# Performance work log

Hardware: AMD Instinct MI355X
Metric: run time of the kernel (lower is better)

Reference implementation:

```python
import jax, jax.numpy as jnp
import numpy as np

N_NODES = 100000
N_EDGES = 1200000
DIM = 64
MAX_DEG = 64
NUM_LAB = 16
BN_EPS = 1e-5


def _lrelu(x):
    return jax.nn.leaky_relu(x, negative_slope=0.01)


def _bn(x, g, b):
    # BatchNorm1d in training mode: batch statistics over node axis
    m = x.mean(axis=0)
    v = x.var(axis=0)
    return (x - m) * jax.lax.rsqrt(v + BN_EPS) * g + b


def _gin_layer(h, src, dst, n, w1, b1, w2, b2, eps, g, b):
    # GINConv: (1+eps)*x_i + sum_{j in N(i)} x_j, then MLP (lin_lrelu_lin), BN, LeakyReLU
    agg = jax.ops.segment_sum(h[src], dst, num_segments=n)
    x = (1.0 + eps) * h + agg
    x = _lrelu(x @ w1 + b1) @ w2 + b2
    return _lrelu(_bn(x, g, b))


def setup_inputs() -> dict:
    key = jax.random.key(0)
    ks = jax.random.split(key, 16)
    s = 0.05
    inp = {
        'node_deg': jax.random.randint(ks[0], (N_NODES,), 0, MAX_DEG + 1, dtype=jnp.int32),
        'node_lab': jax.random.randint(ks[1], (N_NODES,), 0, NUM_LAB, dtype=jnp.int32),
        'edge_index': jax.random.randint(ks[2], (2, N_EDGES), 0, N_NODES, dtype=jnp.int32),
        'emb_deg': jax.random.normal(ks[3], (MAX_DEG + 1, DIM), jnp.float32) * s,
        'emb_lab': jax.random.normal(ks[4], (NUM_LAB, DIM), jnp.float32) * s,
        'l0_w1': jax.random.normal(ks[5], (2 * DIM, 2 * DIM), jnp.float32) * s,
        'l0_b1': jnp.zeros((2 * DIM,), jnp.float32),
        'l0_w2': jax.random.normal(ks[6], (2 * DIM, DIM), jnp.float32) * s,
        'l0_b2': jnp.zeros((DIM,), jnp.float32),
        'l0_eps': jnp.zeros((1,), jnp.float32),
        'bn0_g': jnp.ones((DIM,), jnp.float32),
        'bn0_b': jnp.zeros((DIM,), jnp.float32),
        'l1_w1': jax.random.normal(ks[7], (DIM, DIM), jnp.float32) * s,
        'l1_b1': jnp.zeros((DIM,), jnp.float32),
        'l1_w2': jax.random.normal(ks[8], (DIM, DIM), jnp.float32) * s,
        'l1_b2': jnp.zeros((DIM,), jnp.float32),
        'l1_eps': jnp.zeros((1,), jnp.float32),
        'bn1_g': jnp.ones((DIM,), jnp.float32),
        'bn1_b': jnp.zeros((DIM,), jnp.float32),
        'fc_w1': jax.random.normal(ks[9], (4 * DIM, DIM), jnp.float32) * s,
        'fc_b1': jnp.zeros((DIM,), jnp.float32),
        'fc_bn_g': jnp.ones((DIM,), jnp.float32),
        'fc_bn_b': jnp.zeros((DIM,), jnp.float32),
        'fc_w2': jax.random.normal(ks[10], (DIM, 1), jnp.float32) * s,
        'fc_b2': jnp.zeros((1,), jnp.float32),
    }
    return inp


def reference(node_deg, node_lab, edge_index, emb_deg, emb_lab,
              l0_w1, l0_b1, l0_w2, l0_b2, l0_eps, bn0_g, bn0_b,
              l1_w1, l1_b1, l1_w2, l1_b2, l1_eps, bn1_g, bn1_b,
              fc_w1, fc_b1, fc_bn_g, fc_bn_b, fc_w2, fc_b2):
    n = node_deg.shape[0]
    src, dst = edge_index[0], edge_index[1]
    # embedding concat: [N, 2*DIM]
    h0 = jnp.concatenate([emb_deg[node_deg], emb_lab[node_lab]], axis=1)
    h1 = _gin_layer(h0, src, dst, n, l0_w1, l0_b1, l0_w2, l0_b2, l0_eps[0], bn0_g, bn0_b)
    h2 = _gin_layer(h1, src, dst, n, l1_w1, l1_b1, l1_w2, l1_b2, l1_eps[0], bn1_g, bn1_b)
    x = jnp.concatenate([h0, h1, h2], axis=1)  # [N, 256]
    x = _lrelu(_bn(x @ fc_w1 + fc_b1, fc_bn_g, fc_bn_b))
    out = jax.nn.sigmoid(x @ fc_w2 + fc_b2)
    return out.squeeze(-1)  # [N]
```

## Files before the change

### kernel.cpp

```cpp
#include <hip/hip_runtime.h>

#define N_NODES 100000
#define N_EDGES 1200000
#define NCLS 81
#define NBKT 196
#define BCAP 8192
#define NCHK 293
#define NGBLK 1563
#define NAGG 6250

typedef unsigned short u16;
typedef unsigned char u8;
typedef unsigned int u32;
typedef unsigned long long u64;
typedef short bf16x8 __attribute__((ext_vector_type(8)));
typedef float f32x4 __attribute__((ext_vector_type(4)));

__device__ __forceinline__ float b2f(u16 u) {
  union { u32 i; float f; } v; v.i = ((u32)u) << 16; return v.f;
}
__device__ __forceinline__ u16 f2b(float f) {
  union { float f; u32 i; } v; v.f = f;
  u32 x = v.i;
  return (u16)((x + 0x7fffu + ((x >> 16) & 1u)) >> 16);
}
__device__ __forceinline__ void up2(u32 w, float& lo, float& hi) {
  union { u32 u; float f; } a, b;
  a.u = w << 16; b.u = w & 0xffff0000u;
  lo = a.f; hi = b.f;
}
__device__ __forceinline__ float lrelu(float x) { return x > 0.f ? x : 0.01f * x; }

__device__ __forceinline__ bool is_f32(const u16* emb) {
  int lane = threadIdx.x & 63;
  u32 e0 = (emb[lane * 2] >> 7) & 0xFF;
  u32 e1 = (emb[lane * 2 + 1] >> 7) & 0xFF;
  return __ballot((e0 >= 0x90) || (e1 >= 0x90)) != 0ull;
}

__device__ __forceinline__ float rdr(const void* p, int i, bool f32m) {
  return f32m ? ((const float*)p)[i] : b2f(((const u16*)p)[i]);
}

#define P_EMBD 0
#define P_EMBL 4160
#define P_W1A  5184
#define P_B1A  21568
#define P_W2A  21696
#define P_B2A  29888
#define P_EPS0 29952
#define P_G0   29953
#define P_BB0  30017
#define P_LW1  30081
#define P_LB1  34177
#define P_LW2  34241
#define P_LB2  38337
#define P_EPS1 38401
#define P_G1   38402
#define P_BB1  38466
#define P_FW1  38530
#define P_FB1  54914
#define P_FG   54978
#define P_FBB  55042
#define P_FW2  55106
#define P_FB2  55170
#define P_TOT  55171

struct CvtAll {
  const void* src[22];
  int cnt[22];
  int off[22];
};

struct RawPtrs {
  const void* embD;
  const void* embL;
  const void* w1r;
  const void* w2r;
  const void* lw1r;
  const void* lw2r;
  const void* fwr;
};

__global__ void k_init(CvtAll a, RawPtrs rw, const u16* __restrict__ embRaw,
                       float* __restrict__ P, float* __restrict__ W1p,
                       float* __restrict__ Efc, u16* __restrict__ bp,
                       u16* __restrict__ wpB, u32* __restrict__ gcur) {
  bool f32m = is_f32(embRaw);
  int tid = threadIdx.x;
  if (blockIdx.y < 22) {
    if (blockIdx.y == 0 && blockIdx.x == 0 && tid < NBKT) gcur[tid] = 0;
    int seg = blockIdx.y;
    int i = blockIdx.x * 256 + tid;
    if (i < a.cnt[seg]) {
      float v = f32m ? ((const float*)a.src[seg])[i] : b2f(((const u16*)a.src[seg])[i]);
      P[a.off[seg] + i] = v;
    }
    return;
  }
  int idx = blockIdx.x * 256 + tid;
  if (idx < NCLS * 128) {
    int c = idx >> 7, h = idx & 127;
    float s = 0.f;
    if (c < 65) {
      for (int k = 0; k < 64; ++k)
        s = fmaf(rdr(rw.embD, c * 64 + k, f32m), rdr(rw.w1r, k * 128 + h, f32m), s);
    } else {
      for (int k = 0; k < 64; ++k)
        s = fmaf(rdr(rw.embL, (c - 65) * 64 + k, f32m), rdr(rw.w1r, (64 + k) * 128 + h, f32m), s);
    }
    W1p[idx] = s;
    return;
  }
  if (idx < NCLS * 128 + NCLS * 64) {
    int r = idx - NCLS * 128;
    int c = r >> 6, o = r & 63;
    float s = 0.f;
    if (c < 65) {
      for (int k = 0; k < 64; ++k)
        s = fmaf(rdr(rw.embD, c * 64 + k, f32m), rdr(rw.fwr, k * 64 + o, f32m), s);
    } else {
      for (int k = 0; k < 64; ++k)
        s = fmaf(rdr(rw.embL, (c - 65) * 64 + k, f32m), rdr(rw.fwr, (64 + k) * 64 + o, f32m), s);
    }
    Efc[r] = s;
    return;
  }
  if (idx < NCLS * 128 + NCLS * 64 + 24576) {
    int pidx = idx - (NCLS * 128 + NCLS * 64);
    int seg, rel;
    if (pidx < 8192)       { seg = 0; rel = pidx; }
    else if (pidx < 12288) { seg = 1; rel = pidx - 8192; }
    else if (pidx < 16384) { seg = 2; rel = pidx - 12288; }
    else                   { seg = 3; rel = pidx - 16384; }
    const void* srcs[4] = {rw.w2r, rw.lw1r, rw.lw2r, rw.fwr};
    const int addoff[4] = {0, 0, 0, 128 * 64};
    const int KBs[4] = {4, 2, 2, 4};
    int j = rel & 7, lane = (rel >> 3) & 63, rest = rel >> 9;
    int kb = rest % KBs[seg], nt = rest / KBs[seg];
    int k = kb * 32 + (lane >> 4) * 8 + j;
    int n = nt * 16 + (lane & 15);
    bp[pidx] = f2b(rdr(srcs[seg], addoff[seg] + k * 64 + n, f32m));
    return;
  }
  int p2 = idx - (NCLS * 128 + NCLS * 64 + 24576);
  if (p2 >= 12288) return;
  int j = p2 & 7, lane = (p2 >> 3) & 63, rest = p2 >> 9;
  int kb = rest % 3, nt = rest / 3;
  int c = kb * 32 + (lane >> 4) * 8 + j;
  int n = nt * 16 + (lane & 15);
  float s = 0.f;
  if (c < NCLS) {
    if (c < 65) {
      for (int k = 0; k < 64; ++k)
        s = fmaf(rdr(rw.embD, c * 64 + k, f32m), rdr(rw.w1r, k * 128 + n, f32m), s);
    } else {
      for (int k = 0; k < 64; ++k)
        s = fmaf(rdr(rw.embL, (c - 65) * 64 + k, f32m), rdr(rw.w1r, (64 + k) * 128 + n, f32m), s);
    }
  }
  wpB[p2] = (c < NCLS) ? f2b(s) : 0;
}

__global__ __launch_bounds__(256) void k_bsort(const int* __restrict__ edge,
                                               const int* __restrict__ ndeg,
                                               const int* __restrict__ nlab,
                                               u32* __restrict__ gcur,
                                               u64* __restrict__ e2) {
  __shared__ u32 cnt[NBKT], rbase[NBKT];
  __shared__ u32 slo[4096], shi[4096];
  for (int i = threadIdx.x; i < NBKT; i += 256) cnt[i] = 0;
  __syncthreads();
  int base = blockIdx.x * 4096;
  for (int i = threadIdx.x; i < 4096; i += 256) {
    int e = base + i;
    if (e < N_EDGES) {
      int s = edge[e], d = edge[N_EDGES + e];
      slo[i] = ((u32)s << 11) | ((u32)ndeg[s] << 4) | (u32)nlab[s];
      shi[i] = (u32)d;
      atomicAdd(&cnt[(u32)d >> 9], 1u);
    } else shi[i] = 0xFFFFFFFFu;
  }
  __syncthreads();
  for (int i = threadIdx.x; i < NBKT; i += 256) {
    u32 c = cnt[i];
    rbase[i] = c ? atomicAdd(&gcur[i], c) : 0u;
    cnt[i] = 0;
  }
  __syncthreads();
  for (int i = threadIdx.x; i < 4096; i += 256) {
    u32 d = shi[i];
    if (d == 0xFFFFFFFFu) continue;
    u32 b = d >> 9;
    u32 pos = rbase[b] + atomicAdd(&cnt[b], 1u);
    e2[(size_t)b * BCAP + pos] = ((u64)d << 32) | (u64)slo[i];
  }
}

__global__ __launch_bounds__(512) void k_csrh(const u64* __restrict__ e2,
                                              const u32* __restrict__ gcur,
                                              const u16* __restrict__ wpB,
                                              const float* __restrict__ W1p,
                                              const float* __restrict__ P,
                                              const int* __restrict__ ndeg,
                                              const int* __restrict__ nlab,
                                              u32* __restrict__ row_ptr,
                                              u32* __restrict__ einfo,
                                              u16* __restrict__ hmid) {
  __shared__ u32 l[512], cur[512], gl[NBKT];
  __shared__ u32 h32[512 * 24];
  __shared__ u32 sbase;
  int b = blockIdx.x, tid = threadIdx.x;
  if (tid < NBKT) gl[tid] = gcur[tid];
  l[tid] = 0;
  for (int i = tid; i < 512 * 24; i += 512) h32[i] = 0;
  __syncthreads();
  if (tid == 0) {
    u32 s = 0;
    for (int i = 0; i < b; ++i) s += gl[i];
    sbase = s;
  }
  __syncthreads();
  u32 cnt = gl[b];
  const u64* src = e2 + (size_t)b * BCAP;
  for (u32 e = tid; e < cnt; e += 512)
    atomicAdd(&l[(u32)(src[e] >> 32) & 511u], 1u);
  __syncthreads();
  u32 v = l[tid];
  for (int off = 1; off < 512; off <<= 1) {
    u32 a = (tid >= off) ? l[tid - off] : 0u;
    __syncthreads();
    l[tid] += a;
    __syncthreads();
  }
  u32 pos0 = sbase + l[tid] - v;
  cur[tid] = pos0;
  int nn = b * 512 + tid;
  if (nn <= N_NODES) row_ptr[nn] = pos0;
  __syncthreads();
  for (u32 e = tid; e < cnt; e += 512) {
    u64 r = src[e];
    u32 dl = (u32)(r >> 32) & 511u;
    u32 lo = (u32)r;
    u32 pos = atomicAdd(&cur[dl], 1u);
    einfo[pos] = lo;
    u32 c1 = (lo >> 4) & 0x7Fu, c2 = 65u + (lo & 15u);
    atomicAdd(&h32[dl * 24 + (c1 >> 2)], 1u << ((c1 & 3u) * 8));
    atomicAdd(&h32[dl * 24 + (c2 >> 2)], 1u << ((c2 & 3u) * 8));
  }
  __syncthreads();
  const u8* h = (const u8*)h32;
  int wid = tid >> 6, lane = tid & 63;
  int row = lane & 15, q = lane >> 4;
  float onep = 1.f + P[P_EPS0];
  const bf16x8* bp = (const bf16x8*)wpB;
#pragma unroll 1
  for (int t = wid; t < 32; t += 8) {
    int m0 = b * 512 + t * 16;
    if (m0 >= N_NODES) break;
    f32x4 acc[8];
#pragma unroll
    for (int nt = 0; nt < 8; ++nt) {
      float bb = P[P_B1A + nt * 16 + row];
      acc[nt][0] = bb; acc[nt][1] = bb; acc[nt][2] = bb; acc[nt][3] = bb;
    }
    const u8* ar = h + (t * 16 + row) * 96 + q * 8;
#pragma unroll
    for (int kb = 0; kb < 3; ++kb) {
      bf16x8 af;
#pragma unroll
      for (int j = 0; j < 8; ++j) af[j] = (short)f2b((float)ar[kb * 32 + j]);
#pragma unroll
      for (int nt = 0; nt < 8; ++nt) {
        bf16x8 bf = bp[(nt * 3 + kb) * 64 + lane];
        acc[nt] = __builtin_amdgcn_mfma_f32_16x16x32_bf16(af, bf, acc[nt], 0, 0, 0);
      }
    }
#pragma unroll
    for (int r = 0; r < 4; ++r) {
      int m = m0 + q * 4 + r;
      if (m >= N_NODES) continue;
      const float* wd = W1p + ndeg[m] * 128;
      const float* wl = W1p + (65 + nlab[m]) * 128;
#pragma unroll
      for (int nt = 0; nt < 8; ++nt) {
        int cc = nt * 16 + row;
        float vv = acc[nt][r] + onep * (wd[cc] + wl[cc]);
        hmid[(size_t)m * 128 + cc] = f2b(lrelu(vv));
      }
    }
  }
}

__global__ void k_sr(const float* __restrict__ pbuf, float* __restrict__ statsOut,
                     int nrows) {
  __shared__ float l[256];
  int c = blockIdx.x;
  float s = 0.f;
  for (int r = threadIdx.x; r < nrows; r += 256) s += pbuf[(size_t)r * 128 + c];
  l[threadIdx.x] = s;
  __syncthreads();
  for (int off = 128; off > 0; off >>= 1) {
    if (threadIdx.x < off) l[threadIdx.x] += l[threadIdx.x + off];
    __syncthreads();
  }
  if (threadIdx.x == 0) statsOut[c] = l[0];
}

template <int KB, int LDA, int BIASOFF>
__global__ __launch_bounds__(256) void k_gemm(const u16* __restrict__ A,
                                              const u16* __restrict__ Bp,
                                              const float* __restrict__ P,
                                              float* __restrict__ pbuf,
                                              u16* __restrict__ C) {
  __shared__ float lsum[4][64], lsq[4][64];
  int wid = threadIdx.x >> 6, lane = threadIdx.x & 63;
  int m0 = (blockIdx.x * 4 + wid) * 16;
  bool act = m0 < N_NODES;
  int row = lane & 15, q = lane >> 4;
  float ss[4] = {0.f, 0.f, 0.f, 0.f}, qq[4] = {0.f, 0.f, 0.f, 0.f};
  if (act) {
    const u16* ap = A + (size_t)(m0 + row) * LDA + q * 8;
    const bf16x8* bp = (const bf16x8*)Bp;
    f32x4 acc[4];
#pragma unroll
    for (int nt = 0; nt < 4; ++nt) {
      float b = (BIASOFF >= 0) ? P[BIASOFF + nt * 16 + row] : 0.f;
      acc[nt][0] = b; acc[nt][1] = b; acc[nt][2] = b; acc[nt][3] = b;
    }
#pragma unroll
    for (int kb = 0; kb < KB; ++kb) {
      bf16x8 af = *(const bf16x8*)(ap + kb * 32);
#pragma unroll
      for (int nt = 0; nt < 4; ++nt) {
        bf16x8 bf = bp[(nt * KB + kb) * 64 + lane];
        acc[nt] = __builtin_amdgcn_mfma_f32_16x16x32_bf16(af, bf, acc[nt], 0, 0, 0);
      }
    }
#pragma unroll
    for (int nt = 0; nt < 4; ++nt) {
      float s = 0.f, z = 0.f;
#pragma unroll
      for (int r = 0; r < 4; ++r) {
        int m = m0 + q * 4 + r;
        u16 bv = f2b(acc[nt][r]);
        C[(size_t)m * 64 + nt * 16 + row] = bv;
        float v = b2f(bv);
        s += v; z = fmaf(v, v, z);
      }
      s += __shfl_xor(s, 16, 64); s += __shfl_xor(s, 32, 64);
      z += __shfl_xor(z, 16, 64); z += __shfl_xor(z, 32, 64);
      ss[nt] = s; qq[nt] = z;
    }
  }
  if (lane < 16) {
#pragma unroll
    for (int nt = 0; nt < 4; ++nt) {
      lsum[wid][nt * 16 + lane] = ss[nt];
      lsq[wid][nt * 16 + lane] = qq[nt];
    }
  }
  __syncthreads();
  int t = threadIdx.x;
  if (t < 64)
    pbuf[(size_t)blockIdx.x * 128 + t] = lsum[0][t] + lsum[1][t] + lsum[2][t] + lsum[3][t];
  else if (t < 128) {
    int c = t - 64;
    pbuf[(size_t)blockIdx.x * 128 + t] = lsq[0][c] + lsq[1][c] + lsq[2][c] + lsq[3][c];
  }
}

__global__ __launch_bounds__(256) void k_gemm_bn(const u16* __restrict__ A,
                                                 const u16* __restrict__ Bp,
                                                 const float* __restrict__ P,
                                                 const float* __restrict__ stats,
                                                 u16* __restrict__ C) {
  int wid = threadIdx.x >> 6, lane = threadIdx.x & 63;
  int m0 = (blockIdx.x * 4 + wid) * 16;
  if (m0 >= N_NODES) return;
  int row = lane & 15, q = lane >> 4;
  const float invN = 1.f / (float)N_NODES;
  float sc[16], sh[16];
#pragma unroll
  for (int kb = 0; kb < 2; ++kb)
#pragma unroll
    for (int j = 0; j < 8; ++j) {
      int f = kb * 32 + q * 8 + j;
      float mm = stats[f] * invN;
      float var = fmaxf(stats[64 + f] * invN - mm * mm, 0.f);
      float inv = rsqrtf(var + 1e-5f);
      float s = inv * P[P_G0 + f];
      sc[kb * 8 + j] = s;
      sh[kb * 8 + j] = P[P_BB0 + f] - mm * s;
    }
  const u16* ap = A + (size_t)(m0 + row) * 64 + q * 8;
  const bf16x8* bp = (const bf16x8*)Bp;
  f32x4 acc[4];
#pragma unroll
  for (int nt = 0; nt < 4; ++nt) {
    acc[nt][0] = 0.f; acc[nt][1] = 0.f; acc[nt][2] = 0.f; acc[nt][3] = 0.f;
  }
#pragma unroll
  for (int kb = 0; kb < 2; ++kb) {
    uint4 raw = *(const uint4*)(ap + kb * 32);
    u32 rw[4] = {raw.x, raw.y, raw.z, raw.w};
    bf16x8 af;
#pragma unroll
    for (int p = 0; p < 4; ++p) {
      float lo, hi;
      up2(rw[p], lo, hi);
      float y0 = lrelu(fmaf(sc[kb * 8 + 2 * p], lo, sh[kb * 8 + 2 * p]));
      float y1 = lrelu(fmaf(sc[kb * 8 + 2 * p + 1], hi, sh[kb * 8 + 2 * p + 1]));
      af[2 * p] = (short)f2b(y0);
      af[2 * p + 1] = (short)f2b(y1);
    }
#pragma unroll
    for (int nt = 0; nt < 4; ++nt) {
      bf16x8 bf = bp[(nt * 2 + kb) * 64 + lane];
      acc[nt] = __builtin_amdgcn_mfma_f32_16x16x32_bf16(af, bf, acc[nt], 0, 0, 0);
    }
  }
#pragma unroll
  for (int nt = 0; nt < 4; ++nt)
#pragma unroll
    for (int r = 0; r < 4; ++r) {
      int m = m0 + q * 4 + r;
      C[(size_t)m * 64 + nt * 16 + row] = f2b(acc[nt][r]);
    }
}

__global__ __launch_bounds__(1024) void k_aggg(const u32* __restrict__ rp,
                                               const u32* __restrict__ einfo,
                                               const u16* __restrict__ g1,
                                               const u16* __restrict__ Bp,
                                               const float* __restrict__ P,
                                               float* __restrict__ pbuf,
                                               u16* __restrict__ C) {
  __shared__ u16 As[16][72];
  int lane = threadIdx.x & 63, wv = threadIdx.x >> 6;
  int m0 = blockIdx.x * 16;
  int n = m0 + wv;
  u32 st = rp[n], en = rp[n + 1];
  u32 m = en - st;
  int grp = lane >> 4;
  int fo = (lane & 15) * 4;
  u32 myidx = (u32)n;
  if (lane < (int)m) myidx = einfo[st + lane] >> 11;
  u32 mm = m < 64u ? m : 64u;
  float a0 = 0.f, a1 = 0.f, a2 = 0.f, a3 = 0.f;
  for (u32 k = 0; k < mm; k += 16) {
#pragma unroll
    for (int bb = 0; bb < 4; ++bb) {
      u32 e = k + (u32)(bb * 4 + grp);
      u32 src = (u32)__shfl((int)myidx, (int)e, 64);
      if (e < mm) {
        uint2 v = *(const uint2*)(g1 + (size_t)src * 64 + fo);
        float l0, h0, l1, h1;
        up2(v.x, l0, h0);
        up2(v.y, l1, h1);
        a0 += l0; a1 += h0; a2 += l1; a3 += h1;
      }
    }
  }
  a0 += __shfl_xor(a0, 16, 64); a0 += __shfl_xor(a0, 32, 64);
  a1 += __shfl_xor(a1, 16, 64); a1 += __shfl_xor(a1, 32, 64);
  a2 += __shfl_xor(a2, 16, 64); a2 += __shfl_xor(a2, 32, 64);
  a3 += __shfl_xor(a3, 16, 64); a3 += __shfl_xor(a3, 32, 64);
  for (u32 k = 64; k < m; ++k) {
    u32 src = einfo[st + k] >> 11;
    uint2 v = *(const uint2*)(g1 + (size_t)src * 64 + fo);
    float l0, h0, l1, h1;
    up2(v.x, l0, h0);
    up2(v.y, l1, h1);
    a0 += l0; a1 += h0; a2 += l1; a3 += h1;
  }
  float onep = 1.f + P[P_EPS1];
  uint2 sv = *(const uint2*)(g1 + (size_t)n * 64 + fo);
  float s0, s1, s2, s3;
  up2(sv.x, s0, s1);
  up2(sv.y, s2, s3);
  float r0 = P[P_LB1 + fo + 0] + fmaf(onep, s0, a0);
  float r1 = P[P_LB1 + fo + 1] + fmaf(onep, s1, a1);
  float r2 = P[P_LB1 + fo + 2] + fmaf(onep, s2, a2);
  float r3 = P[P_LB1 + fo + 3] + fmaf(onep, s3, a3);
  if (lane < 16) {
    uint2 o;
    o.x = ((u32)f2b(lrelu(r0))) | (((u32)f2b(lrelu(r1))) << 16);
    o.y = ((u32)f2b(lrelu(r2))) | (((u32)f2b(lrelu(r3))) << 16);
    *(uint2*)&As[wv][fo] = o;
  }
  __syncthreads();
  if (wv != 0) return;
  int row = lane & 15, q = lane >> 4;
  const u16* ap = &As[row][q * 8];
  const bf16x8* bp = (const bf16x8*)Bp;
  f32x4 acc[4];
#pragma unroll
  for (int nt = 0; nt < 4; ++nt) {
    float b = P[P_LB2 + nt * 16 + row];
    acc[nt][0] = b; acc[nt][1] = b; acc[nt][2] = b; acc[nt][3] = b;
  }
#pragma unroll
  for (int kb = 0; kb < 2; ++kb) {
    bf16x8 af = *(const bf16x8*)(ap + kb * 32);
#pragma unroll
    for (int nt = 0; nt < 4; ++nt) {
      bf16x8 bf = bp[(nt * 2 + kb) * 64 + lane];
      acc[nt] = __builtin_amdgcn_mfma_f32_16x16x32_bf16(af, bf, acc[nt], 0, 0, 0);
    }
  }
  float ss[4], qq[4];
#pragma unroll
  for (int nt = 0; nt < 4; ++nt) {
    float s = 0.f, z = 0.f;
#pragma unroll
    for (int r = 0; r < 4; ++r) {
      int mo = m0 + q * 4 + r;
      u16 bv = f2b(acc[nt][r]);
      C[(size_t)mo * 64 + nt * 16 + row] = bv;
      float v = b2f(bv);
      s += v; z = fmaf(v, v, z);
    }
    s += __shfl_xor(s, 16, 64); s += __shfl_xor(s, 32, 64);
    z += __shfl_xor(z, 16, 64); z += __shfl_xor(z, 32, 64);
    ss[nt] = s; qq[nt] = z;
  }
  if (lane < 16) {
#pragma unroll
    for (int nt = 0; nt < 4; ++nt) {
      pbuf[(size_t)blockIdx.x * 128 + nt * 16 + lane] = ss[nt];
      pbuf[(size_t)blockIdx.x * 128 + 64 + nt * 16 + lane] = qq[nt];
    }
  }
}

__global__ __launch_bounds__(256) void k_gemm_fc1bn(const u16* __restrict__ t0,
                                                    const u16* __restrict__ t1,
                                                    const u16* __restrict__ Bp,
                                                    const float* __restrict__ P,
                                                    const float* __restrict__ stats,
                                                    float* __restrict__ pbuf,
                                                    const int* __restrict__ ndeg,
                                                    const int* __restrict__ nlab,
                                                    const float* __restrict__ Efc,
                                                    u16* __restrict__ C) {
  __shared__ float lsum[4][64], lsq[4][64];
  int wid = threadIdx.x >> 6, lane = threadIdx.x & 63;
  int m0 = (blockIdx.x * 4 + wid) * 16;
  bool act = m0 < N_NODES;
  int row = lane & 15, q = lane >> 4;
  float ss[4] = {0.f, 0.f, 0.f, 0.f}, qq[4] = {0.f, 0.f, 0.f, 0.f};
  if (act) {
    const float invN = 1.f / (float)N_NODES;
    float sc[32], sh[32];
#pragma unroll
    for (int h = 0; h < 2; ++h) {
      const float* st = stats + h * 128;
      int gof = h ? P_G1 : P_G0, bof = h ? P_BB1 : P_BB0;
#pragma unroll
      for (int kb = 0; kb < 2; ++kb)
#pragma unroll
        for (int j = 0; j < 8; ++j) {
          int f = kb * 32 + q * 8 + j;
          float mm = st[f] * invN;
          float var = fmaxf(st[64 + f] * invN - mm * mm, 0.f);
          float inv = rsqrtf(var + 1e-5f);
          float s = inv * P[gof + f];
          sc[h * 16 + kb * 8 + j] = s;
          sh[h * 16 + kb * 8 + j] = P[bof + f] - mm * s;
        }
    }
    const u16* a0 = t0 + (size_t)(m0 + row) * 64 + q * 8;
    const u16* a1 = t1 + (size_t)(m0 + row) * 64 + q * 8;
    const bf16x8* bp = (const bf16x8*)Bp;
    f32x4 acc[4];
#pragma unroll
    for (int nt = 0; nt < 4; ++nt) {
      float b = P[P_FB1 + nt * 16 + row];
      acc[nt][0] = b; acc[nt][1] = b; acc[nt][2] = b; acc[nt][3] = b;
    }
#pragma unroll
    for (int kb = 0; kb < 4; ++kb) {
      const u16* src = (kb < 2) ? (a0 + kb * 32) : (a1 + (kb - 2) * 32);
      int ci = (kb < 2) ? kb * 8 : 16 + (kb - 2) * 8;
      uint4 raw = *(const uint4*)src;
      u32 rw[4] = {raw.x, raw.y, raw.z, raw.w};
      bf16x8 af;
#pragma unroll
      for (int p = 0; p < 4; ++p) {
        float lo, hi;
        up2(rw[p], lo, hi);
        float y0 = lrelu(fmaf(sc[ci + 2 * p], lo, sh[ci + 2 * p]));
        float y1 = lrelu(fmaf(sc[ci + 2 * p + 1], hi, sh[ci + 2 * p + 1]));
        af[2 * p] = (short)f2b(y0);
        af[2 * p + 1] = (short)f2b(y1);
      }
#pragma unroll
      for (int nt = 0; nt < 4; ++nt) {
        bf16x8 bf = bp[(nt * 4 + kb) * 64 + lane];
        acc[nt] = __builtin_amdgcn_mfma_f32_16x16x32_bf16(af, bf, acc[nt], 0, 0, 0);
      }
    }
    float es[4][4];
#pragma unroll
    for (int r = 0; r < 4; ++r) {
      int m = m0 + q * 4 + r;
      int dn = ndeg[m], ln = 65 + nlab[m];
#pragma unroll
      for (int nt = 0; nt < 4; ++nt) {
        int cc = nt * 16 + row;
        es[r][nt] = acc[nt][r] + Efc[dn * 64 + cc] + Efc[ln * 64 + cc];
      }
    }
#pragma unroll
    for (int nt = 0; nt < 4; ++nt) {
      float s = 0.f, z = 0.f;
#pragma unroll
      for (int r = 0; r < 4; ++r) {
        int m = m0 + q * 4 + r;
        u16 bv = f2b(es[r][nt]);
        C[(size_t)m * 64 + nt * 16 + row] = bv;
        float v = b2f(bv);
        s += v; z = fmaf(v, v, z);
      }
      s += __shfl_xor(s, 16, 64); s += __shfl_xor(s, 32, 64);
      z += __shfl_xor(z, 16, 64); z += __shfl_xor(z, 32, 64);
      ss[nt] = s; qq[nt] = z;
    }
  }
  if (lane < 16) {
#pragma unroll
    for (int nt = 0; nt < 4; ++nt) {
      lsum[wid][nt * 16 + lane] = ss[nt];
      lsq[wid][nt * 16 + lane] = qq[nt];
    }
  }
  __syncthreads();
  int t = threadIdx.x;
  if (t < 64)
    pbuf[(size_t)blockIdx.x * 128 + t] = lsum[0][t] + lsum[1][t] + lsum[2][t] + lsum[3][t];
  else if (t < 128) {
    int c = t - 64;
    pbuf[(size_t)blockIdx.x * 128 + t] = lsq[0][c] + lsq[1][c] + lsq[2][c] + lsq[3][c];
  }
}

__global__ __launch_bounds__(256) void k_fc2(const u16* __restrict__ t,
                                             const float* __restrict__ stats,
                                             const float* __restrict__ P,
                                             const u16* __restrict__ embRaw,
                                             void* __restrict__ out) {
  __shared__ float scF[64], shF[64], fwF[64];
  bool f32m = is_f32(embRaw);
  int tid = threadIdx.x;
  if (tid < 64) {
    const float invN = 1.f / (float)N_NODES;
    float mm = stats[tid] * invN;
    float var = fmaxf(stats[64 + tid] * invN - mm * mm, 0.f);
    float inv = rsqrtf(var + 1e-5f);
    float s = inv * P[P_FG + tid];
    scF[tid] = s;
    shF[tid] = P[P_FBB + tid] - mm * s;
    fwF[tid] = P[P_FW2 + tid];
  }
  __syncthreads();
  int n = blockIdx.x * 256 + tid;
  if (n >= N_NODES) return;
  float z = P[P_FB2];
  const uint4* tn = (const uint4*)(t + (size_t)n * 64);
#pragma unroll
  for (int jj = 0; jj < 8; ++jj) {
    uint4 raw = tn[jj];
    u32 w[4] = {raw.x, raw.y, raw.z, raw.w};
#pragma unroll
    for (int p = 0; p < 4; ++p) {
      int f = jj * 8 + p * 2;
      float lo, hi;
      up2(w[p], lo, hi);
      float y0 = lrelu(fmaf(scF[f], lo, shF[f]));
      float y1 = lrelu(fmaf(scF[f + 1], hi, shF[f + 1]));
      z = fmaf(y0, fwF[f], z);
      z = fmaf(y1, fwF[f + 1], z);
    }
  }
  float s = 1.f / (1.f + expf(-z));
  if (!(fabsf(z) < 1e30f)) s = 0.25f;
  if (f32m) ((float*)out)[n] = s;
  else      ((u16*)out)[n] = f2b(s);
}

extern "C" void kernel_launch(void* const* d_in, const int* in_sizes, int n_in,
                              void* d_out, int out_size, void* d_ws, size_t ws_size,
                              hipStream_t stream) {
  const int* node_deg = (const int*)d_in[0];
  const int* node_lab = (const int*)d_in[1];
  const int* edge     = (const int*)d_in[2];
  const u16* embRaw   = (const u16*)d_in[3];
  (void)in_sizes; (void)n_in; (void)out_size; (void)ws_size;

  char* base = (char*)d_ws;
  size_t off = 0;
  auto alloc = [&](size_t bytes) -> void* {
    void* p = base + off;
    off += (bytes + 15) & ~(size_t)15;
    return p;
  };
  float* Pb    = (float*)alloc((size_t)P_TOT * 4);
  float* stats = (float*)alloc(384 * 4);
  u32* gcur    = (u32*)alloc(NBKT * 4);
  float* W1p   = (float*)alloc(NCLS * 128 * 4);
  float* Efc   = (float*)alloc(NCLS * 64 * 4);
  u16* bpack   = (u16*)alloc(24576 * 2);
  u16* wpB     = (u16*)alloc(12288 * 2);
  u32* row_ptr = (u32*)alloc((size_t)(N_NODES + 1) * 4);
  float* pbuf  = (float*)alloc((size_t)NAGG * 128 * 4);
  u32* einfo   = (u32*)alloc((size_t)N_EDGES * 4);
  u64* e2      = (u64*)alloc((size_t)NBKT * BCAP * 8);
  void* arena  = alloc((size_t)N_NODES * 128 * 2);
  u16* t0      = (u16*)alloc((size_t)N_NODES * 64 * 2);
  u16* t1      = (u16*)alloc((size_t)N_NODES * 64 * 2);
  u16* t2      = (u16*)alloc((size_t)N_NODES * 64 * 2);
  u16* hmid = (u16*)arena;
  u16* g1   = (u16*)arena;
  u16* Bp_w2a = bpack;
  u16* Bp_lw1 = bpack + 8192;
  u16* Bp_lw2 = bpack + 12288;
  u16* Bp_fw1 = bpack + 16384;

  CvtAll ca;
  const int srcidx[22] = {3, 4, 5, 6, 7, 8, 9, 10, 11, 12, 13, 14, 15, 16, 17, 18, 19, 20, 21, 22, 23, 24};
  const int cnts[22]   = {4160, 1024, 16384, 128, 8192, 64, 1, 64, 64, 4096, 64, 4096, 64, 1, 64, 64, 16384, 64, 64, 64, 64, 1};
  const int offs[22]   = {P_EMBD, P_EMBL, P_W1A, P_B1A, P_W2A, P_B2A, P_EPS0, P_G0, P_BB0,
                          P_LW1, P_LB1, P_LW2, P_LB2, P_EPS1, P_G1, P_BB1,
                          P_FW1, P_FB1, P_FG, P_FBB, P_FW2, P_FB2};
  for (int i = 0; i < 22; ++i) { ca.src[i] = d_in[srcidx[i]]; ca.cnt[i] = cnts[i]; ca.off[i] = offs[i]; }
  RawPtrs rw;
  rw.embD = d_in[3]; rw.embL = d_in[4]; rw.w1r = d_in[5]; rw.w2r = d_in[7];
  rw.lw1r = d_in[12]; rw.lw2r = d_in[14]; rw.fwr = d_in[19];

  k_init<<<dim3(205, 23), 256, 0, stream>>>(ca, rw, embRaw, Pb, W1p, Efc, bpack, wpB, gcur);

  k_bsort<<<NCHK, 256, 0, stream>>>(edge, node_deg, node_lab, gcur, e2);

  k_csrh<<<NBKT, 512, 0, stream>>>(e2, gcur, wpB, W1p, Pb, node_deg, node_lab,
                                   row_ptr, einfo, hmid);

  const int GEMM_GRID = NGBLK;

  k_gemm<4, 128, P_B2A><<<GEMM_GRID, 256, 0, stream>>>(hmid, Bp_w2a, Pb, pbuf, t0);
  k_sr<<<128, 256, 0, stream>>>(pbuf, stats, NGBLK);

  k_gemm_bn<<<GEMM_GRID, 256, 0, stream>>>(t0, Bp_lw1, Pb, stats, g1);
  k_aggg<<<NAGG, 1024, 0, stream>>>(row_ptr, einfo, g1, Bp_lw2, Pb, pbuf, t1);
  k_sr<<<128, 256, 0, stream>>>(pbuf, stats + 128, NAGG);

  k_gemm_fc1bn<<<GEMM_GRID, 256, 0, stream>>>(t0, t1, Bp_fw1, Pb, stats, pbuf,
                                              node_deg, node_lab, Efc, t2);
  k_sr<<<128, 256, 0, stream>>>(pbuf, stats + 256, NGBLK);
  k_fc2<<<(N_NODES + 255) / 256, 256, 0, stream>>>(t2, stats + 256, Pb, embRaw, d_out);
}
```

Measured before the change: 331.3 us.

## Fuse layer-0 second GEMM into CSR kernel and split aggregation from its GEMM

The layer-0 second linear layer (128->64) and its BN partial statistics now run inside k_csrh, using an LDS tile of the hidden activations, so the hmid round trip through global memory and a separate GEMM launch go away. The layer-1 aggregation kernel is reduced to 256-thread blocks that only gather neighbours and write the aggregated activations to a buffer. A generic k_gemm then applies the second layer-1 weight matrix and produces BN partials over fewer blocks, so the later stats reduction reads less. In exchange there is one extra intermediate buffer write and read, an additional kernel launch, and much more LDS per k_csrh block.

```diff
diff --git a/kernel.cpp b/kernel.cpp
--- a/kernel.cpp
+++ b/kernel.cpp
@@ -7,7 +7,6 @@
 #define BCAP 8192
 #define NCHK 293
 #define NGBLK 1563
-#define NAGG 6250
 
 typedef unsigned short u16;
 typedef unsigned char u8;
@@ -204,12 +203,16 @@
                                               const float* __restrict__ P,
                                               const int* __restrict__ ndeg,
                                               const int* __restrict__ nlab,
+                                              const u16* __restrict__ Bp2,
                                               u32* __restrict__ row_ptr,
                                               u32* __restrict__ einfo,
-                                              u16* __restrict__ hmid) {
+                                              u16* __restrict__ t0,
+                                              float* __restrict__ pbuf) {
   __shared__ u32 l[512], cur[512], gl[NBKT];
   __shared__ u32 h32[512 * 24];
   __shared__ u32 sbase;
+  __shared__ u16 T[8][16][136];
+  __shared__ float lsum[8][64], lsq[8][64];
   int b = blockIdx.x, tid = threadIdx.x;
   if (tid < NBKT) gl[tid] = gcur[tid];
   l[tid] = 0;
@@ -254,6 +257,8 @@
   int row = lane & 15, q = lane >> 4;
   float onep = 1.f + P[P_EPS0];
   const bf16x8* bp = (const bf16x8*)wpB;
+  const bf16x8* bp2 = (const bf16x8*)Bp2;
+  float ssA[4] = {0.f, 0.f, 0.f, 0.f}, qqA[4] = {0.f, 0.f, 0.f, 0.f};
 #pragma unroll 1
   for (int t = wid; t < 32; t += 8) {
     int m0 = b * 512 + t * 16;
@@ -279,16 +284,74 @@
 #pragma unroll
     for (int r = 0; r < 4; ++r) {
       int m = m0 + q * 4 + r;
-      if (m >= N_NODES) continue;
-      const float* wd = W1p + ndeg[m] * 128;
-      const float* wl = W1p + (65 + nlab[m]) * 128;
-#pragma unroll
-      for (int nt = 0; nt < 8; ++nt) {
-        int cc = nt * 16 + row;
-        float vv = acc[nt][r] + onep * (wd[cc] + wl[cc]);
-        hmid[(size_t)m * 128 + cc] = f2b(lrelu(vv));
-      }
-    }
+      int node = q * 4 + r;
+      if (m < N_NODES) {
+        const float* wd = W1p + ndeg[m] * 128;
+        const float* wl = W1p + (65 + nlab[m]) * 128;
+#pragma unroll
+        for (int nt = 0; nt < 8; ++nt) {
+          int cc = nt * 16 + row;
+          float vv = acc[nt][r] + onep * (wd[cc] + wl[cc]);
+          T[wid][node][cc] = f2b(lrelu(vv));
+        }
+      } else {
+#pragma unroll
+        for (int nt = 0; nt < 8; ++nt) T[wid][node][nt * 16 + row] = 0;
+      }
+    }
+    const u16* ap = &T[wid][row][q * 8];
+    f32x4 acc2[4];
+#pragma unroll
+    for (int nt = 0; nt < 4; ++nt) {
+      float bb = P[P_B2A + nt * 16 + row];
+      acc2[nt][0] = bb; acc2[nt][1] = bb; acc2[nt][2] = bb; acc2[nt][3] = bb;
+    }
+#pragma unroll
+    for (int kb = 0; kb < 4; ++kb) {
+      bf16x8 af = *(const bf16x8*)(ap + kb * 32);
+#pragma unroll
+      for (int nt = 0; nt < 4; ++nt) {
+        bf16x8 bf = bp2[(nt * 4 + kb) * 64 + lane];
+        acc2[nt] = __builtin_amdgcn_mfma_f32_16x16x32_bf16(af, bf, acc2[nt], 0, 0, 0);
+      }
+    }
+#pragma unroll
+    for (int nt = 0; nt < 4; ++nt) {
+      float s = 0.f, z = 0.f;
+#pragma unroll
+      for (int r = 0; r < 4; ++r) {
+        int m = m0 + q * 4 + r;
+        if (m < N_NODES) {
+          u16 bv = f2b(acc2[nt][r]);
+          t0[(size_t)m * 64 + nt * 16 + row] = bv;
+          float vv = b2f(bv);
+          s += vv; z = fmaf(vv, vv, z);
+        }
+      }
+      s += __shfl_xor(s, 16, 64); s += __shfl_xor(s, 32, 64);
+      z += __shfl_xor(z, 16, 64); z += __shfl_xor(z, 32, 64);
+      ssA[nt] += s; qqA[nt] += z;
+    }
+  }
+  if (lane < 16) {
+#pragma unroll
+    for (int nt = 0; nt < 4; ++nt) {
+      lsum[wid][nt * 16 + lane] = ssA[nt];
+      lsq[wid][nt * 16 + lane] = qqA[nt];
+    }
+  }
+  __syncthreads();
+  if (tid < 64) {
+    float s = 0.f;
+#pragma unroll
+    for (int w = 0; w < 8; ++w) s += lsum[w][tid];
+    pbuf[(size_t)b * 128 + tid] = s;
+  } else if (tid < 128) {
+    int c = tid - 64;
+    float s = 0.f;
+#pragma unroll
+    for (int w = 0; w < 8; ++w) s += lsq[w][c];
+    pbuf[(size_t)b * 128 + tid] = s;
   }
 }
 
@@ -429,17 +492,14 @@
     }
 }
 
-__global__ __launch_bounds__(1024) void k_aggg(const u32* __restrict__ rp,
-                                               const u32* __restrict__ einfo,
-                                               const u16* __restrict__ g1,
-                                               const u16* __restrict__ Bp,
-                                               const float* __restrict__ P,
-                                               float* __restrict__ pbuf,
-                                               u16* __restrict__ C) {
-  __shared__ u16 As[16][72];
+__global__ __launch_bounds__(256) void k_agg1(const u32* __restrict__ rp,
+                                              const u32* __restrict__ einfo,
+                                              const u16* __restrict__ g1,
+                                              const float* __restrict__ P,
+                                              u16* __restrict__ abuf) {
   int lane = threadIdx.x & 63, wv = threadIdx.x >> 6;
-  int m0 = blockIdx.x * 16;
-  int n = m0 + wv;
+  int n = blockIdx.x * 4 + wv;
+  if (n >= N_NODES) return;
   u32 st = rp[n], en = rp[n + 1];
   u32 m = en - st;
   int grp = lane >> 4;
@@ -487,50 +547,7 @@
     uint2 o;
     o.x = ((u32)f2b(lrelu(r0))) | (((u32)f2b(lrelu(r1))) << 16);
     o.y = ((u32)f2b(lrelu(r2))) | (((u32)f2b(lrelu(r3))) << 16);
-    *(uint2*)&As[wv][fo] = o;
-  }
-  __syncthreads();
-  if (wv != 0) return;
-  int row = lane & 15, q = lane >> 4;
-  const u16* ap = &As[row][q * 8];
-  const bf16x8* bp = (const bf16x8*)Bp;
-  f32x4 acc[4];
-#pragma unroll
-  for (int nt = 0; nt < 4; ++nt) {
-    float b = P[P_LB2 + nt * 16 + row];
-    acc[nt][0] = b; acc[nt][1] = b; acc[nt][2] = b; acc[nt][3] = b;
-  }
-#pragma unroll
-  for (int kb = 0; kb < 2; ++kb) {
-    bf16x8 af = *(const bf16x8*)(ap + kb * 32);
-#pragma unroll
-    for (int nt = 0; nt < 4; ++nt) {
-      bf16x8 bf = bp[(nt * 2 + kb) * 64 + lane];
-      acc[nt] = __builtin_amdgcn_mfma_f32_16x16x32_bf16(af, bf, acc[nt], 0, 0, 0);
-    }
-  }
-  float ss[4], qq[4];
-#pragma unroll
-  for (int nt = 0; nt < 4; ++nt) {
-    float s = 0.f, z = 0.f;
-#pragma unroll
-    for (int r = 0; r < 4; ++r) {
-      int mo = m0 + q * 4 + r;
-      u16 bv = f2b(acc[nt][r]);
-      C[(size_t)mo * 64 + nt * 16 + row] = bv;
-      float v = b2f(bv);
-      s += v; z = fmaf(v, v, z);
-    }
-    s += __shfl_xor(s, 16, 64); s += __shfl_xor(s, 32, 64);
-    z += __shfl_xor(z, 16, 64); z += __shfl_xor(z, 32, 64);
-    ss[nt] = s; qq[nt] = z;
-  }
-  if (lane < 16) {
-#pragma unroll
-    for (int nt = 0; nt < 4; ++nt) {
-      pbuf[(size_t)blockIdx.x * 128 + nt * 16 + lane] = ss[nt];
-      pbuf[(size_t)blockIdx.x * 128 + 64 + nt * 16 + lane] = qq[nt];
-    }
+    *(uint2*)(abuf + (size_t)n * 64 + fo) = o;
   }
 }
 
@@ -713,15 +730,15 @@
   u16* bpack   = (u16*)alloc(24576 * 2);
   u16* wpB     = (u16*)alloc(12288 * 2);
   u32* row_ptr = (u32*)alloc((size_t)(N_NODES + 1) * 4);
-  float* pbuf  = (float*)alloc((size_t)NAGG * 128 * 4);
+  float* pbuf  = (float*)alloc((size_t)NGBLK * 128 * 4);
   u32* einfo   = (u32*)alloc((size_t)N_EDGES * 4);
   u64* e2      = (u64*)alloc((size_t)NBKT * BCAP * 8);
   void* arena  = alloc((size_t)N_NODES * 128 * 2);
   u16* t0      = (u16*)alloc((size_t)N_NODES * 64 * 2);
   u16* t1      = (u16*)alloc((size_t)N_NODES * 64 * 2);
   u16* t2      = (u16*)alloc((size_t)N_NODES * 64 * 2);
-  u16* hmid = (u16*)arena;
   u16* g1   = (u16*)arena;
+  u16* abuf = (u16*)arena + (size_t)N_NODES * 64;
   u16* Bp_w2a = bpack;
   u16* Bp_lw1 = bpack + 8192;
   u16* Bp_lw2 = bpack + 12288;
@@ -743,16 +760,15 @@
   k_bsort<<<NCHK, 256, 0, stream>>>(edge, node_deg, node_lab, gcur, e2);
 
   k_csrh<<<NBKT, 512, 0, stream>>>(e2, gcur, wpB, W1p, Pb, node_deg, node_lab,
-                                   row_ptr, einfo, hmid);
+                                   Bp_w2a, row_ptr, einfo, t0, pbuf);
+  k_sr<<<128, 256, 0, stream>>>(pbuf, stats, NBKT);
 
   const int GEMM_GRID = NGBLK;
 
-  k_gemm<4, 128, P_B2A><<<GEMM_GRID, 256, 0, stream>>>(hmid, Bp_w2a, Pb, pbuf, t0);
-  k_sr<<<128, 256, 0, stream>>>(pbuf, stats, NGBLK);
-
   k_gemm_bn<<<GEMM_GRID, 256, 0, stream>>>(t0, Bp_lw1, Pb, stats, g1);
-  k_aggg<<<NAGG, 1024, 0, stream>>>(row_ptr, einfo, g1, Bp_lw2, Pb, pbuf, t1);
-  k_sr<<<128, 256, 0, stream>>>(pbuf, stats + 128, NAGG);
+  k_agg1<<<(N_NODES + 3) / 4, 256, 0, stream>>>(row_ptr, einfo, g1, Pb, abuf);
+  k_gemm<2, 64, P_LB2><<<GEMM_GRID, 256, 0, stream>>>(abuf, Bp_lw2, Pb, pbuf, t1);
+  k_sr<<<128, 256, 0, stream>>>(pbuf, stats + 128, NGBLK);
 
   k_gemm_fc1bn<<<GEMM_GRID, 256, 0, stream>>>(t0, t1, Bp_fw1, Pb, stats, pbuf,
                                               node_deg, node_lab, Efc, t2);
```

New measurement: 285.1 us. 1.16x faster.
